# Kernel tuning notes

Hardware: AMD Instinct MI355X
Metric: run time of the kernel (lower is better)

Reference implementation:

```python
import jax, jax.numpy as jnp
import numpy as np

K_SIZE = 5  # must match init_kwargs


def _local_attention(main, ref, ref_value, k_size=K_SIZE):
    """k x k windowed dot-product attention ('dot' mode of RefLocal).

    main:      [B,H,W,C] queries
    ref:       [B,H,W,C] keys (zero-padded SAME, matching extract_volume_patches)
    ref_value: [B,H,W,V] values
    Zero padding contributes logit 0 (NOT -inf), faithful to TF SAME padding.
    """
    p = (k_size - 1) // 2
    B, H, W, C = main.shape
    ref_p = jnp.pad(ref, ((0, 0), (p, p), (p, p), (0, 0)))
    val_p = jnp.pad(ref_value, ((0, 0), (p, p), (p, p), (0, 0)))

    offsets = [(i, j) for i in range(k_size) for j in range(k_size)]
    # logits[b,h,w,idx] = <main[b,h,w,:], ref shifted by offset idx>
    logits = jnp.stack(
        [jnp.einsum('bhwc,bhwc->bhw', main, ref_p[:, i:i + H, j:j + W, :])
         for (i, j) in offsets], axis=-1)  # [B,H,W,k*k]
    attn = jax.nn.softmax(logits, axis=-1)

    out = jnp.zeros(ref_value.shape, dtype=ref_value.dtype)
    for idx, (i, j) in enumerate(offsets):
        out = out + attn[..., idx][..., None] * val_p[:, i:i + H, j:j + W, :]
    return out  # [B,H,W,V]


def setup_inputs() -> dict:
    key = jax.random.key(0)
    k1, k2, k3 = jax.random.split(key, 3)
    B, H, W, C, V = 8, 96, 96, 192, 96
    return {
        'main': jax.random.normal(k1, (B, H, W, C), dtype=jnp.float32),
        'ref': jax.random.normal(k2, (B, H, W, C), dtype=jnp.float32),
        'ref_value': jax.random.normal(k3, (B, H, W, V), dtype=jnp.float32),
    }


def reference(main, ref, ref_value):
    return _local_attention(main, ref, ref_value, K_SIZE)
```

## Files before the change

### kernel.cpp

```cpp
#include <hip/hip_runtime.h>


#define BATCH 8
#define HH 96
#define WW 96
#define CH 192
#define VV 96
#define KS 5
#define PAD 2
#define TH 8
#define TW 8
#define HT (TH + 2 * PAD)
#define WT (TW + 2 * PAD)
#define NPIX (HT * WT)
#define CHUNK 32
#define SPX 36
#define SO 36
#define SOFF (NPIX * SPX)
#define SSZ (SOFF + 64 * SO)

#define DOT4(m, k) \
  ((m).x * (k).x + (m).y * (k).y + (m).z * (k).z + (m).w * (k).w)

__global__ __launch_bounds__(256, 2) void reflocal_kernel(
    const float* __restrict__ qry, const float* __restrict__ key,
    const float* __restrict__ val, float* __restrict__ out) {
  int braw = blockIdx.x;
  int L = (braw & 7) * 144 + (braw >> 3);
  int bb = L / 144;
  int t2 = L - bb * 144;
  int tyy = t2 / 12;
  int txx = t2 - tyy * 12;
  int h0 = tyy * TH, w0 = txx * TW;

  int tid = threadIdx.x;
  int s4 = (tid & 7) * 4;
  int pr = (tid >> 3) >> 2;
  int pc = (tid >> 3) & 3;
  int qx0 = 2 * pc;

  __shared__ float s[SSZ];

  int pidx[5];
  int ldst[5];
#pragma unroll
  for (int r = 0; r < 5; ++r) {
    int px = (tid >> 3) + 32 * r;
    if (px < NPIX) {
      int ry = px / WT, rx = px - ry * WT;
      int hh = h0 - PAD + ry, ww = w0 - PAD + rx;
      pidx[r] = ((unsigned)hh < HH && (unsigned)ww < WW)
                    ? (bb * HH + hh) * WW + ww
                    : -1;
      ldst[r] = px * SPX + s4;
    } else {
      pidx[r] = -2;
      ldst[r] = 0;
    }
  }

  float lg0[25], lg1[25];
#pragma unroll
  for (int o = 0; o < 25; ++o) { lg0[o] = 0.f; lg1[o] = 0.f; }

  const float* qb0 =
      qry + (size_t)((bb * HH + h0 + pr) * WW + w0 + qx0) * CH;
  const float* qb1 = qb0 + CH;

  float4 pf[5];
#pragma unroll
  for (int r = 0; r < 5; ++r) {
    float4 v4 = make_float4(0.f, 0.f, 0.f, 0.f);
    if (pidx[r] >= 0)
      v4 = *(const float4*)(key + (size_t)pidx[r] * CH + s4);
    pf[r] = v4;
  }

  for (int c0 = 0; c0 < CH; c0 += CHUNK) {
    __syncthreads();
#pragma unroll
    for (int r = 0; r < 5; ++r)
      if (pidx[r] != -2) *(float4*)(&s[ldst[r]]) = pf[r];
    __syncthreads();
    if (c0 + CHUNK < CH) {
      int cn = c0 + CHUNK + s4;
#pragma unroll
      for (int r = 0; r < 5; ++r) {
        float4 v4 = make_float4(0.f, 0.f, 0.f, 0.f);
        if (pidx[r] >= 0)
          v4 = *(const float4*)(key + (size_t)pidx[r] * CH + cn);
        pf[r] = v4;
      }
    }

    float4 m0 = *(const float4*)(qb0 + c0 + s4);
    float4 m1 = *(const float4*)(qb1 + c0 + s4);
#pragma unroll
    for (int i = 0; i < KS; ++i) {
      const float* sp = &s[((pr + i) * WT + qx0) * SPX + s4];
      float4 kr[6];
#pragma unroll
      for (int u = 0; u < 6; ++u) kr[u] = *(const float4*)(sp + u * SPX);
#pragma unroll
      for (int j = 0; j < KS; ++j) {
        lg0[i * 5 + j] += DOT4(m0, kr[j]);
        lg1[i * 5 + j] += DOT4(m1, kr[j + 1]);
      }
    }
  }

#pragma unroll
  for (int o = 0; o < 25; ++o) {
    lg0[o] += __shfl_xor(lg0[o], 1);
    lg0[o] += __shfl_xor(lg0[o], 2);
    lg0[o] += __shfl_xor(lg0[o], 4);
    lg1[o] += __shfl_xor(lg1[o], 1);
    lg1[o] += __shfl_xor(lg1[o], 2);
    lg1[o] += __shfl_xor(lg1[o], 4);
  }

#pragma unroll
  for (int r = 0; r < 5; ++r) {
    float4 v4 = make_float4(0.f, 0.f, 0.f, 0.f);
    if (pidx[r] >= 0)
      v4 = *(const float4*)(val + (size_t)pidx[r] * VV + s4);
    pf[r] = v4;
  }

  {
    float mx = lg0[0];
#pragma unroll
    for (int o = 1; o < 25; ++o) mx = fmaxf(mx, lg0[o]);
    float sum = 0.f;
#pragma unroll
    for (int o = 0; o < 25; ++o) {
      lg0[o] = __expf(lg0[o] - mx);
      sum += lg0[o];
    }
    float inv = 1.f / sum;
#pragma unroll
    for (int o = 0; o < 25; ++o) lg0[o] *= inv;
  }
  {
    float mx = lg1[0];
#pragma unroll
    for (int o = 1; o < 25; ++o) mx = fmaxf(mx, lg1[o]);
    float sum = 0.f;
#pragma unroll
    for (int o = 0; o < 25; ++o) {
      lg1[o] = __expf(lg1[o] - mx);
      sum += lg1[o];
    }
    float inv = 1.f / sum;
#pragma unroll
    for (int o = 0; o < 25; ++o) lg1[o] *= inv;
  }

  for (int v0 = 0; v0 < VV; v0 += CHUNK) {
    __syncthreads();
#pragma unroll
    for (int r = 0; r < 5; ++r)
      if (pidx[r] != -2) *(float4*)(&s[ldst[r]]) = pf[r];
    __syncthreads();
    if (v0 + CHUNK < VV) {
      int vn = v0 + CHUNK + s4;
#pragma unroll
      for (int r = 0; r < 5; ++r) {
        float4 v4 = make_float4(0.f, 0.f, 0.f, 0.f);
        if (pidx[r] >= 0)
          v4 = *(const float4*)(val + (size_t)pidx[r] * VV + vn);
        pf[r] = v4;
      }
    }

    float4 a0 = make_float4(0.f, 0.f, 0.f, 0.f);
    float4 a1 = make_float4(0.f, 0.f, 0.f, 0.f);
#pragma unroll
    for (int i = 0; i < KS; ++i) {
      const float* sp = &s[((pr + i) * WT + qx0) * SPX + s4];
      float4 vr[6];
#pragma unroll
      for (int u = 0; u < 6; ++u) vr[u] = *(const float4*)(sp + u * SPX);
#pragma unroll
      for (int j = 0; j < KS; ++j) {
        float w0a = lg0[i * 5 + j];
        float w1a = lg1[i * 5 + j];
        a0.x += w0a * vr[j].x;     a0.y += w0a * vr[j].y;
        a0.z += w0a * vr[j].z;     a0.w += w0a * vr[j].w;
        a1.x += w1a * vr[j + 1].x; a1.y += w1a * vr[j + 1].y;
        a1.z += w1a * vr[j + 1].z; a1.w += w1a * vr[j + 1].w;
      }
    }
    int px0 = pr * 8 + qx0;
    *(float4*)(&s[SOFF + px0 * SO + s4]) = a0;
    *(float4*)(&s[SOFF + (px0 + 1) * SO + s4]) = a1;
    __syncthreads();

    for (int t = tid; t < 64 * (CHUNK / 4); t += 256) {
      int px = t >> 3, c4 = (t & 7) * 4;
      int pty = px >> 3, ptx = px & 7;
      float4 v4 = *(const float4*)(&s[SOFF + px * SO + c4]);
      *(float4*)(out + (size_t)((bb * HH + h0 + pty) * WW + w0 + ptx) * VV +
                 v0 + c4) = v4;
    }
  }
}

extern "C" void kernel_launch(void* const* d_in, const int* in_sizes, int n_in,
                              void* d_out, int out_size, void* d_ws,
                              size_t ws_size, hipStream_t stream) {
  const float* qry = (const float*)d_in[0];
  const float* key = (const float*)d_in[1];
  const float* val = (const float*)d_in[2];
  float* out = (float*)d_out;

  dim3 grid(BATCH * (HH / TH) * (WW / TW));
  dim3 block(256);
  reflocal_kernel<<<grid, block, 0, stream>>>(qry, key, val, out);
}
```

Before: 210.5 us.

## Double-buffer LDS with direct global-to-LDS async loads for key/value tiles

Replaces the register-staged prefetch (global load into registers, then store to shared) with __builtin_amdgcn_global_load_lds writes straight into two alternating LDS buffers. The next key chunk, or the first value chunk, is issued before the current chunk is computed, and one barrier per iteration is dropped. Padding pixels are zero-filled once in both buffers. In exchange the row stride loses its padding (SPX 36 to 32), which may add LDS bank conflicts, and shared memory use grows. Correctness relies on the compiler waiting for the async LDS writes to finish before each barrier.

```diff
diff --git a/kernel.cpp b/kernel.cpp
--- a/kernel.cpp
+++ b/kernel.cpp
@@ -14,13 +14,20 @@
 #define WT (TW + 2 * PAD)
 #define NPIX (HT * WT)
 #define CHUNK 32
-#define SPX 36
+#define SPX 32
+#define BUFSZ (NPIX * SPX)
 #define SO 36
-#define SOFF (NPIX * SPX)
+#define SOFF (2 * BUFSZ)
 #define SSZ (SOFF + 64 * SO)
 
 #define DOT4(m, k) \
   ((m).x * (k).x + (m).y * (k).y + (m).z * (k).z + (m).w * (k).w)
+
+__device__ __forceinline__ void gload16(const float* g, float* l) {
+  __builtin_amdgcn_global_load_lds(
+      (const __attribute__((address_space(1))) float*)g,
+      (__attribute__((address_space(3))) float*)l, 16, 0, 0);
+}
 
 __global__ __launch_bounds__(256, 2) void reflocal_kernel(
     const float* __restrict__ qry, const float* __restrict__ key,
@@ -38,11 +45,11 @@
   int pr = (tid >> 3) >> 2;
   int pc = (tid >> 3) & 3;
   int qx0 = 2 * pc;
+  int wv = tid >> 6;
 
   __shared__ float s[SSZ];
 
   int pidx[5];
-  int ldst[5];
 #pragma unroll
   for (int r = 0; r < 5; ++r) {
     int px = (tid >> 3) + 32 * r;
@@ -52,10 +59,18 @@
       pidx[r] = ((unsigned)hh < HH && (unsigned)ww < WW)
                     ? (bb * HH + hh) * WW + ww
                     : -1;
-      ldst[r] = px * SPX + s4;
     } else {
       pidx[r] = -2;
-      ldst[r] = 0;
+    }
+  }
+
+#pragma unroll
+  for (int r = 0; r < 5; ++r) {
+    if (pidx[r] == -1) {
+      int px = (tid >> 3) + 32 * r;
+      float4 z = make_float4(0.f, 0.f, 0.f, 0.f);
+      *(float4*)(&s[px * SPX + s4]) = z;
+      *(float4*)(&s[BUFSZ + px * SPX + s4]) = z;
     }
   }
 
@@ -67,37 +82,37 @@
       qry + (size_t)((bb * HH + h0 + pr) * WW + w0 + qx0) * CH;
   const float* qb1 = qb0 + CH;
 
-  float4 pf[5];
-#pragma unroll
-  for (int r = 0; r < 5; ++r) {
-    float4 v4 = make_float4(0.f, 0.f, 0.f, 0.f);
-    if (pidx[r] >= 0)
-      v4 = *(const float4*)(key + (size_t)pidx[r] * CH + s4);
-    pf[r] = v4;
-  }
-
-  for (int c0 = 0; c0 < CH; c0 += CHUNK) {
+  auto stage = [&](float* buf, const float* src, int rl, int c0) {
+#pragma unroll
+    for (int r = 0; r < 5; ++r) {
+      int pxs = 32 * r + 8 * wv;
+      if (pxs < NPIX) {
+        if (pidx[r] >= 0)
+          gload16(src + pidx[r] * rl + c0 + s4, buf + pxs * SPX);
+      }
+    }
+  };
+
+  float* const bufA = (float*)s;
+  float* const bufB = (float*)s + BUFSZ;
+
+  stage(bufA, key, CH, 0);
+
+  for (int ci = 0; ci < CH / CHUNK; ++ci) {
     __syncthreads();
-#pragma unroll
-    for (int r = 0; r < 5; ++r)
-      if (pidx[r] != -2) *(float4*)(&s[ldst[r]]) = pf[r];
-    __syncthreads();
-    if (c0 + CHUNK < CH) {
-      int cn = c0 + CHUNK + s4;
-#pragma unroll
-      for (int r = 0; r < 5; ++r) {
-        float4 v4 = make_float4(0.f, 0.f, 0.f, 0.f);
-        if (pidx[r] >= 0)
-          v4 = *(const float4*)(key + (size_t)pidx[r] * CH + cn);
-        pf[r] = v4;
-      }
-    }
-
+    float* cur = (ci & 1) ? bufB : bufA;
+    float* nxt = (ci & 1) ? bufA : bufB;
+    if (ci + 1 < CH / CHUNK)
+      stage(nxt, key, CH, (ci + 1) * CHUNK);
+    else
+      stage(nxt, val, VV, 0);
+
+    int c0 = ci * CHUNK;
     float4 m0 = *(const float4*)(qb0 + c0 + s4);
     float4 m1 = *(const float4*)(qb1 + c0 + s4);
 #pragma unroll
     for (int i = 0; i < KS; ++i) {
-      const float* sp = &s[((pr + i) * WT + qx0) * SPX + s4];
+      const float* sp = &cur[((pr + i) * WT + qx0) * SPX + s4];
       float4 kr[6];
 #pragma unroll
       for (int u = 0; u < 6; ++u) kr[u] = *(const float4*)(sp + u * SPX);
@@ -119,14 +134,6 @@
     lg1[o] += __shfl_xor(lg1[o], 4);
   }
 
-#pragma unroll
-  for (int r = 0; r < 5; ++r) {
-    float4 v4 = make_float4(0.f, 0.f, 0.f, 0.f);
-    if (pidx[r] >= 0)
-      v4 = *(const float4*)(val + (size_t)pidx[r] * VV + s4);
-    pf[r] = v4;
-  }
-
   {
     float mx = lg0[0];
 #pragma unroll
@@ -156,28 +163,17 @@
     for (int o = 0; o < 25; ++o) lg1[o] *= inv;
   }
 
-  for (int v0 = 0; v0 < VV; v0 += CHUNK) {
+  for (int vi = 0; vi < VV / CHUNK; ++vi) {
     __syncthreads();
-#pragma unroll
-    for (int r = 0; r < 5; ++r)
-      if (pidx[r] != -2) *(float4*)(&s[ldst[r]]) = pf[r];
-    __syncthreads();
-    if (v0 + CHUNK < VV) {
-      int vn = v0 + CHUNK + s4;
-#pragma unroll
-      for (int r = 0; r < 5; ++r) {
-        float4 v4 = make_float4(0.f, 0.f, 0.f, 0.f);
-        if (pidx[r] >= 0)
-          v4 = *(const float4*)(val + (size_t)pidx[r] * VV + vn);
-        pf[r] = v4;
-      }
-    }
+    float* cur = (vi & 1) ? bufB : bufA;
+    float* nxt = (vi & 1) ? bufA : bufB;
+    if (vi + 1 < VV / CHUNK) stage(nxt, val, VV, (vi + 1) * CHUNK);
 
     float4 a0 = make_float4(0.f, 0.f, 0.f, 0.f);
     float4 a1 = make_float4(0.f, 0.f, 0.f, 0.f);
 #pragma unroll
     for (int i = 0; i < KS; ++i) {
-      const float* sp = &s[((pr + i) * WT + qx0) * SPX + s4];
+      const float* sp = &cur[((pr + i) * WT + qx0) * SPX + s4];
       float4 vr[6];
 #pragma unroll
       for (int u = 0; u < 6; ++u) vr[u] = *(const float4*)(sp + u * SPX);
@@ -196,6 +192,7 @@
     *(float4*)(&s[SOFF + (px0 + 1) * SO + s4]) = a1;
     __syncthreads();
 
+    int v0 = vi * CHUNK;
     for (int t = tid; t < 64 * (CHUNK / 4); t += 256) {
       int px = t >> 3, c4 = (t & 7) * 4;
       int pty = px >> 3, ptx = px & 7;
```

Result: faster. 189.6 us (-9.9%).
